# Optimization experiments

Hardware: AMD Instinct MI355X
Metric: run time of the kernel (lower is better)

The kernel has to match this reference:

```python
import jax, jax.numpy as jnp
import numpy as np

EPS = 1e-6


def _layernorm2d(x, w, b):
    # Normalize over channel dim (axis=1) per pixel; x: [B,C,H,W]
    mu = jnp.mean(x, axis=1, keepdims=True)
    var = jnp.var(x, axis=1, keepdims=True)
    xn = (x - mu) * jax.lax.rsqrt(var + EPS)
    return xn * w[None, :, None, None] + b[None, :, None, None]


def _conv1x1(x, w, b):
    # 1x1 conv == channel matmul; w: [Cout, Cin], x: [B,Cin,H,W]
    return jnp.einsum('oc,bchw->bohw', w, x) + b[None, :, None, None]


def setup_inputs() -> dict:
    key = jax.random.key(0)
    ks = jax.random.split(key, 8)
    B, C, H, W = 4, 64, 180, 320
    s = C ** -0.5  # keep projection weights at sane scale
    return {
        'x_l': jax.random.normal(ks[0], (B, C, H, W), jnp.float32),
        'x_r': jax.random.normal(ks[1], (B, C, H, W), jnp.float32),
        'ln_l_w': jnp.ones((C,), jnp.float32),
        'ln_l_b': jnp.zeros((C,), jnp.float32),
        'ln_r_w': jnp.ones((C,), jnp.float32),
        'ln_r_b': jnp.zeros((C,), jnp.float32),
        'wq_l': jax.random.normal(ks[2], (C, C), jnp.float32) * s,
        'bq_l': jnp.zeros((C,), jnp.float32),
        'wq_r': jax.random.normal(ks[3], (C, C), jnp.float32) * s,
        'bq_r': jnp.zeros((C,), jnp.float32),
        'wv_l': jax.random.normal(ks[4], (C, C), jnp.float32) * s,
        'bv_l': jnp.zeros((C,), jnp.float32),
        'wv_r': jax.random.normal(ks[5], (C, C), jnp.float32) * s,
        'bv_r': jnp.zeros((C,), jnp.float32),
        'beta': jax.random.normal(ks[6], (C,), jnp.float32) * 0.1,
        'gamma': jax.random.normal(ks[7], (C,), jnp.float32) * 0.1,
    }


def reference(x_l, x_r, ln_l_w, ln_l_b, ln_r_w, ln_r_b,
              wq_l, bq_l, wq_r, bq_r, wv_l, bv_l, wv_r, bv_r,
              beta, gamma):
    C = x_l.shape[1]
    scale = C ** -0.5
    # Q projections of LayerNorm'd inputs (Select stub == identity pass-through)
    Q_l = _conv1x1(_layernorm2d(x_l, ln_l_w, ln_l_b), wq_l, bq_l)  # [B,C,H,W]
    Q_r = _conv1x1(_layernorm2d(x_r, ln_r_w, ln_r_b), wq_r, bq_r)  # [B,C,H,W]
    V_l = _conv1x1(x_l, wv_l, bv_l)  # [B,C,H,W]
    V_r = _conv1x1(x_r, wv_r, bv_r)  # [B,C,H,W]
    # attention over width per row: [B,H,Wl,Wr]
    attn = jnp.einsum('bchw,bchv->bhwv', Q_l, Q_r) * scale
    # r -> l: softmax over Wr (last axis), contract with V_r
    F_r2l = jnp.einsum('bhwv,bchv->bchw', jax.nn.softmax(attn, axis=-1), V_r)
    # l -> r: softmax over Wl (axis=2 of attn), contract with V_l
    F_l2r = jnp.einsum('bhwv,bchw->bchv', jax.nn.softmax(attn, axis=2), V_l)
    out_l = x_l + F_r2l * beta[None, :, None, None]
    out_r = x_r + F_l2r * gamma[None, :, None, None]
    return (out_l, out_r)
```

## Files before the change

kernel.cpp:

```cpp
#include <hip/hip_runtime.h>


#define HWs  57600
#define CHWs 3686400
#define TOTs 14745600
#define RST  72
#define VST  328
#define PTS  36
#define NTH  768

typedef short bf16x8 __attribute__((ext_vector_type(8)));
typedef float f32x4  __attribute__((ext_vector_type(4)));
union FragU { uint4 q; unsigned short u[8]; bf16x8 v; };

__device__ __forceinline__ unsigned short f2bf(float f) {
  unsigned u = __float_as_uint(f);
  u += 0x7fffu + ((u >> 16) & 1u);
  return (unsigned short)(u >> 16);
}
__device__ __forceinline__ float bf2f(unsigned short s) {
  return __uint_as_float(((unsigned)s) << 16);
}
__device__ __forceinline__ unsigned fenc(float f) {
  unsigned u = __float_as_uint(f);
  return u ^ (0x80000000u | (unsigned)(-(int)(u >> 31)));
}
__device__ __forceinline__ float fdec(unsigned k) {
  return __uint_as_float(k ^ (0x80000000u | (unsigned)(-(int)((k >> 31) ^ 1u))));
}

__global__ __launch_bounds__(NTH, 2)
void sfam_kernel(
    const float* __restrict__ x_l, const float* __restrict__ x_r,
    const float* __restrict__ ln_l_w, const float* __restrict__ ln_l_b,
    const float* __restrict__ ln_r_w, const float* __restrict__ ln_r_b,
    const float* __restrict__ wq_l, const float* __restrict__ bq_l,
    const float* __restrict__ wq_r, const float* __restrict__ bq_r,
    const float* __restrict__ wv_l, const float* __restrict__ bv_l,
    const float* __restrict__ wv_r, const float* __restrict__ bv_r,
    const float* __restrict__ beta, const float* __restrict__ gamma,
    float* __restrict__ out)
{
  __shared__ __align__(16) unsigned short Rs[320*RST];
  __shared__ __align__(16) unsigned short Ks[320*RST];
  __shared__ __align__(16) unsigned short Vb[64*VST];
  __shared__ __align__(16) unsigned short Pt[12*16*PTS];
  __shared__ float NX[320];
  __shared__ float MU[640], RSd[640];
  __shared__ float c_arr[320];
  __shared__ float BB[128];
  __shared__ unsigned SCu[3];

  const int bh = blockIdx.x;
  const int b = bh / 180, h = bh - b*180;
  const int base = b*CHWs + h*320;

  const int t = threadIdx.x;
  const int wave = t >> 6, lane = t & 63;
  const int p = lane & 15, g = lane >> 4;
  const int nwt = (wave < 8) ? 2 : 1;
  const int w0 = (wave < 8) ? wave*32 : 256 + (wave-8)*16;

  if (t < 3) SCu[t] = 0u;

  for (int w2 = t; w2 < 640; w2 += NTH) {
    const int side = (w2 >= 320);
    const int w = w2 - side*320;
    const float* xp = side ? x_r : x_l;
    unsigned short* dst = side ? Ks : Rs;
    float s0 = 0.f, q0 = 0.f, s1 = 0.f, q1 = 0.f;
    #pragma unroll
    for (int cb = 0; cb < 64; cb += 8) {
      FragU f;
      #pragma unroll
      for (int j = 0; j < 8; ++j) {
        const float v = xp[base + (cb+j)*HWs + w];
        if (cb < 32) { s0 += v; q0 += v*v; } else { s1 += v; q1 += v*v; }
        f.u[j] = f2bf(v);
      }
      *(uint4*)&dst[w*RST + cb] = f.q;
    }
    const float m  = (s0 + s1) * (1.f/64.f);
    const float vv = (q0 + q1) * (1.f/64.f) - m*m;
    MU[side*320 + w]  = m;
    RSd[side*320 + w] = rsqrtf(vv + 1e-6f);
    if (side) {
      const float vc = fmaxf(vv, 0.f);
      const float nx = 8.f * sqrtf(vc / (vc + 1e-6f));
      NX[w] = nx;
      atomicMax(&SCu[0], fenc(nx));
    }
  }
  if (t < 128) {
    const int o = t & 63;
    const float* wqp = (t < 64) ? wq_l : wq_r;
    const float* lwp = (t < 64) ? ln_l_w : ln_r_w;
    const float* lbp = (t < 64) ? ln_l_b : ln_r_b;
    const float* bqp = (t < 64) ? bq_l : bq_r;
    float s = bqp[o];
    for (int c = 0; c < 64; ++c) s += wqp[o*64+c]*lwp[c]*lbp[c];
    BB[t] = s;
  }
  __syncthreads();

  auto projV = [&](const float* wvp, const float* bvp, const unsigned short* src,
                   const float* mup, const float* rsp, bool inv) {
    bf16x8 bx[2][2];
    #pragma unroll
    for (int nt = 0; nt < 2; ++nt) if (nt < nwt) {
      const int w = w0 + nt*16 + p;
      const float mu = mup[w];
      const float sd = inv ? (1.0f / rsp[w]) : 0.f;
      #pragma unroll
      for (int kf = 0; kf < 2; ++kf) {
        FragU f; f.q = *(const uint4*)&src[w*RST + kf*32 + g*8];
        if (inv) {
          FragU rr;
          #pragma unroll
          for (int j = 0; j < 8; ++j) rr.u[j] = f2bf(bf2f(f.u[j])*sd + mu);
          bx[nt][kf] = rr.v;
        } else bx[nt][kf] = f.v;
      }
    }
    #pragma unroll
    for (int mt = 0; mt < 4; ++mt) {
      bf16x8 av2[2];
      #pragma unroll
      for (int kf = 0; kf < 2; ++kf) {
        FragU rr;
        #pragma unroll
        for (int j = 0; j < 8; ++j) rr.u[j] = f2bf(wvp[(mt*16+p)*64 + kf*32 + g*8 + j]);
        av2[kf] = rr.v;
      }
      f32x4 acc2[2];
      #pragma unroll
      for (int nt = 0; nt < 2; ++nt) acc2[nt] = (f32x4){0.f,0.f,0.f,0.f};
      #pragma unroll
      for (int nt = 0; nt < 2; ++nt) if (nt < nwt)
        #pragma unroll
        for (int kf = 0; kf < 2; ++kf)
          acc2[nt] = __builtin_amdgcn_mfma_f32_16x16x32_bf16(av2[kf], bx[nt][kf], acc2[nt], 0,0,0);
      #pragma unroll
      for (int nt = 0; nt < 2; ++nt) if (nt < nwt)
        #pragma unroll
        for (int r = 0; r < 4; ++r) {
          const int o = mt*16 + g*4 + r;
          Vb[o*VST + w0 + nt*16 + p] = f2bf(acc2[nt][r] + bvp[o]);
        }
    }
  };

  projV(wv_l, bv_l, Rs, MU, RSd, false);

  float cR[2][4];
  {
    bf16x8 qa[2][2];
    #pragma unroll
    for (int wt = 0; wt < 2; ++wt) if (wt < nwt) {
      const int w = w0 + wt*16 + p;
      const float mu = MU[w], rs = RSd[w];
      #pragma unroll
      for (int kf = 0; kf < 2; ++kf) {
        FragU f; f.q = *(const uint4*)&Rs[w*RST + kf*32 + g*8];
        FragU rr;
        #pragma unroll
        for (int j = 0; j < 8; ++j) rr.u[j] = f2bf((bf2f(f.u[j]) - mu) * rs);
        qa[wt][kf] = rr.v;
      }
    }
    f32x4 qacc[2][4];
    #pragma unroll
    for (int wt = 0; wt < 2; ++wt)
      #pragma unroll
      for (int ot = 0; ot < 4; ++ot) qacc[wt][ot] = (f32x4){0.f,0.f,0.f,0.f};
    #pragma unroll
    for (int ot = 0; ot < 4; ++ot) {
      bf16x8 bw2[2];
      #pragma unroll
      for (int kf = 0; kf < 2; ++kf) {
        FragU rr;
        #pragma unroll
        for (int j = 0; j < 8; ++j) {
          const int c = kf*32 + g*8 + j;
          rr.u[j] = f2bf(wq_l[(ot*16+p)*64 + c] * ln_l_w[c]);
        }
        bw2[kf] = rr.v;
      }
      #pragma unroll
      for (int wt = 0; wt < 2; ++wt) if (wt < nwt)
        #pragma unroll
        for (int kf = 0; kf < 2; ++kf)
          qacc[wt][ot] = __builtin_amdgcn_mfma_f32_16x16x32_bf16(qa[wt][kf], bw2[kf], qacc[wt][ot], 0,0,0);
    }
    #pragma unroll
    for (int wt = 0; wt < 2; ++wt) {
      #pragma unroll
      for (int r = 0; r < 4; ++r) cR[wt][r] = 0.f;
      if (wt < nwt) {
        #pragma unroll
        for (int ot = 0; ot < 4; ++ot) {
          const float bl = BB[ot*16+p], br = BB[64 + ot*16+p];
          #pragma unroll
          for (int r = 0; r < 4; ++r) {
            const float qv = qacc[wt][ot][r] + bl;
            Rs[(w0 + wt*16 + g*4 + r)*RST + ot*16 + p] = f2bf(qv);
            cR[wt][r] += qv * br;
          }
        }
        #pragma unroll
        for (int r = 0; r < 4; ++r) {
          float cv = cR[wt][r];
          cv += __shfl_xor(cv, 1); cv += __shfl_xor(cv, 2);
          cv += __shfl_xor(cv, 4); cv += __shfl_xor(cv, 8);
          cv *= 0.125f;
          cR[wt][r] = cv;
          if (p == 0) {
            c_arr[w0 + wt*16 + g*4 + r] = cv;
            atomicMax(&SCu[2], fenc(cv));
          }
        }
      }
    }
  }

  float rm[2][4];
  {
    bf16x8 qla[2][2];
    #pragma unroll
    for (int wt = 0; wt < 2; ++wt) if (wt < nwt)
      #pragma unroll
      for (int kf = 0; kf < 2; ++kf) {
        FragU f; f.q = *(const uint4*)&Rs[(w0 + wt*16 + p)*RST + kf*32 + g*8];
        qla[wt][kf] = f.v;
      }
    f32x4 q2[2][4];
    #pragma unroll
    for (int wt = 0; wt < 2; ++wt)
      #pragma unroll
      for (int ct = 0; ct < 4; ++ct) q2[wt][ct] = (f32x4){0.f,0.f,0.f,0.f};
    #pragma unroll
    for (int ct = 0; ct < 4; ++ct) {
      const float lw = ln_r_w[ct*16 + p];
      bf16x8 bwt2[2];
      #pragma unroll
      for (int kf = 0; kf < 2; ++kf) {
        FragU rr;
        #pragma unroll
        for (int j = 0; j < 8; ++j)
          rr.u[j] = f2bf(wq_r[(kf*32 + g*8 + j)*64 + ct*16 + p] * lw);
        bwt2[kf] = rr.v;
      }
      #pragma unroll
      for (int wt = 0; wt < 2; ++wt) if (wt < nwt)
        #pragma unroll
        for (int kf = 0; kf < 2; ++kf)
          q2[wt][ct] = __builtin_amdgcn_mfma_f32_16x16x32_bf16(qla[wt][kf], bwt2[kf], q2[wt][ct], 0,0,0);
    }
    const float NXmax = fdec(SCu[0]);
    #pragma unroll
    for (int wt = 0; wt < 2; ++wt) {
      #pragma unroll
      for (int r = 0; r < 4; ++r) rm[wt][r] = 0.f;
      if (wt < nwt) {
        #pragma unroll
        for (int r = 0; r < 4; ++r) {
          float qsq = 0.f;
          #pragma unroll
          for (int ct = 0; ct < 4; ++ct) {
            const float qv = q2[wt][ct][r] * 0.125f;
            Rs[(w0 + wt*16 + g*4 + r)*RST + ct*16 + p] = f2bf(qv);
            qsq += qv*qv;
          }
          qsq += __shfl_xor(qsq, 1); qsq += __shfl_xor(qsq, 2);
          qsq += __shfl_xor(qsq, 4); qsq += __shfl_xor(qsq, 8);
          rm[wt][r] = sqrtf(qsq) * NXmax;
          if (p == 0) atomicMax(&SCu[1], fenc(qsq));
        }
      }
    }
  }

  #pragma unroll
  for (int wt = 0; wt < 2; ++wt) if (wt < nwt) {
    const int w = w0 + wt*16 + p;
    const float mu = MU[320+w], rs = RSd[320+w];
    #pragma unroll
    for (int kf = 0; kf < 2; ++kf) {
      FragU f; f.q = *(const uint4*)&Ks[w*RST + kf*32 + g*8];
      FragU rr;
      #pragma unroll
      for (int j = 0; j < 8; ++j) rr.u[j] = f2bf((bf2f(f.u[j]) - mu) * rs);
      *(uint4*)&Ks[w*RST + kf*32 + g*8] = rr.q;
    }
  }
  __syncthreads();

  bf16x8 aq[2][2];
  #pragma unroll
  for (int wt = 0; wt < 2; ++wt) if (wt < nwt)
    #pragma unroll
    for (int kf = 0; kf < 2; ++kf) {
      FragU f1; f1.q = *(const uint4*)&Rs[(w0 + wt*16 + p)*RST + kf*32 + g*8];
      aq[wt][kf] = f1.v;
    }

  float ls[2][4];
  f32x4 oacc[2][4];
  auto attn_pass = [&](bf16x8 (&A)[2][2], const unsigned short* Bsrc,
                       float (&mx)[2][4], bool colc) {
    float rsa[2][4];
    #pragma unroll
    for (int wt = 0; wt < 2; ++wt)
      #pragma unroll
      for (int r = 0; r < 4; ++r) rsa[wt][r] = 0.f;
    unsigned short* ptw = &Pt[wave*16*PTS];
    for (int ch = 0; ch < 5; ++ch) {
      const int k0 = ch*64;
      #pragma unroll
      for (int pvk = 0; pvk < 2; ++pvk) {
        bf16x8 bq2[2][2];
        #pragma unroll
        for (int vh = 0; vh < 2; ++vh)
          #pragma unroll
          for (int kf = 0; kf < 2; ++kf) {
            FragU f; f.q = *(const uint4*)&Bsrc[(k0 + (pvk*2+vh)*16 + p)*RST + kf*32 + g*8];
            bq2[vh][kf] = f.v;
          }
        float cc2[2];
        #pragma unroll
        for (int vh = 0; vh < 2; ++vh)
          cc2[vh] = colc ? c_arr[k0 + (pvk*2+vh)*16 + p] : 0.f;
        f32x4 sa[2][2];
        #pragma unroll
        for (int wt = 0; wt < 2; ++wt)
          #pragma unroll
          for (int vh = 0; vh < 2; ++vh) sa[wt][vh] = (f32x4){0.f,0.f,0.f,0.f};
        #pragma unroll
        for (int wt = 0; wt < 2; ++wt) if (wt < nwt)
          #pragma unroll
          for (int vh = 0; vh < 2; ++vh)
            #pragma unroll
            for (int kf = 0; kf < 2; ++kf)
              sa[wt][vh] = __builtin_amdgcn_mfma_f32_16x16x32_bf16(A[wt][kf], bq2[vh][kf], sa[wt][vh], 0,0,0);
        #pragma unroll
        for (int wt = 0; wt < 2; ++wt) if (wt < nwt) {
          #pragma unroll
          for (int r = 0; r < 4; ++r) {
            #pragma unroll
            for (int vh = 0; vh < 2; ++vh) {
              const float e = __expf(sa[wt][vh][r] + cc2[vh] - mx[wt][r]);
              sa[wt][vh][r] = e;
              rsa[wt][r] += e;
            }
          }
        }
        bf16x8 bvv[4];
        #pragma unroll
        for (int ot = 0; ot < 4; ++ot) {
          FragU f; f.q = *(const uint4*)&Vb[(ot*16+p)*VST + k0 + pvk*32 + g*8];
          bvv[ot] = f.v;
        }
        #pragma unroll
        for (int wt = 0; wt < 2; ++wt) if (wt < nwt) {
          #pragma unroll
          for (int vh = 0; vh < 2; ++vh)
            #pragma unroll
            for (int r = 0; r < 4; ++r)
              ptw[(g*4 + r)*PTS + vh*16 + p] = f2bf(sa[wt][vh][r]);
          FragU fa; fa.q = *(const uint4*)&ptw[p*PTS + g*8];
          #pragma unroll
          for (int ot = 0; ot < 4; ++ot)
            oacc[wt][ot] = __builtin_amdgcn_mfma_f32_16x16x32_bf16(fa.v, bvv[ot], oacc[wt][ot], 0,0,0);
        }
      }
    }
    #pragma unroll
    for (int wt = 0; wt < 2; ++wt)
      #pragma unroll
      for (int r = 0; r < 4; ++r) {
        float s = rsa[wt][r];
        s += __shfl_xor(s, 1); s += __shfl_xor(s, 2);
        s += __shfl_xor(s, 4); s += __shfl_xor(s, 8);
        ls[wt][r] = s;
      }
  };

  bf16x8 ak[2][2];
  #pragma unroll
  for (int wt = 0; wt < 2; ++wt) if (wt < nwt)
    #pragma unroll
    for (int kf = 0; kf < 2; ++kf) {
      FragU f2; f2.q = *(const uint4*)&Ks[(w0 + wt*16 + p)*RST + kf*32 + g*8];
      ak[wt][kf] = f2.v;
    }
  float cmR[2][4];
  {
    const float Qnmax = sqrtf(fdec(SCu[1]));
    const float Cmax  = fdec(SCu[2]);
    #pragma unroll
    for (int wt = 0; wt < 2; ++wt)
      #pragma unroll
      for (int r = 0; r < 4; ++r)
        cmR[wt][r] = (wt < nwt) ? NX[w0 + wt*16 + g*4 + r] * Qnmax + Cmax : 0.f;
  }
  #pragma unroll
  for (int wt = 0; wt < 2; ++wt)
    #pragma unroll
    for (int ot = 0; ot < 4; ++ot) oacc[wt][ot] = (f32x4){0.f,0.f,0.f,0.f};
  attn_pass(ak, Rs, cmR, true);
  __syncthreads();

  #pragma unroll
  for (int wt = 0; wt < 2; ++wt) if (wt < nwt)
    #pragma unroll
    for (int r = 0; r < 4; ++r) {
      const float inv = 1.0f / ls[wt][r];
      #pragma unroll
      for (int ot = 0; ot < 4; ++ot)
        Rs[(w0 + wt*16 + g*4 + r)*RST + ot*16 + p] = f2bf(oacc[wt][ot][r] * inv);
    }

  projV(wv_r, bv_r, Ks, MU+320, RSd+320, true);
  __syncthreads();

  #pragma unroll
  for (int wt = 0; wt < 2; ++wt)
    #pragma unroll
    for (int ot = 0; ot < 4; ++ot) oacc[wt][ot] = (f32x4){0.f,0.f,0.f,0.f};
  attn_pass(aq, Ks, rm, false);
  __syncthreads();

  #pragma unroll
  for (int wt = 0; wt < 2; ++wt) if (wt < nwt)
    #pragma unroll
    for (int r = 0; r < 4; ++r) {
      const float inv = 1.0f / ls[wt][r];
      #pragma unroll
      for (int ot = 0; ot < 4; ++ot)
        Ks[(w0 + wt*16 + g*4 + r)*RST + ot*16 + p] = f2bf(oacc[wt][ot][r] * inv);
    }
  __syncthreads();

  for (int w2 = t; w2 < 640; w2 += NTH) {
    const int side = (w2 >= 320);
    const int w = w2 - side*320;
    const float* xs = side ? x_r : x_l;
    const unsigned short* Osrc = side ? Rs : Ks;
    const float* sc = side ? gamma : beta;
    float* op = out + (side ? TOTs : 0);
    #pragma unroll
    for (int cb = 0; cb < 64; cb += 8) {
      FragU f; f.q = *(const uint4*)&Osrc[w*RST + cb];
      #pragma unroll
      for (int j = 0; j < 8; ++j) {
        const int cc = cb + j;
        const int gi = base + cc*HWs + w;
        op[gi] = xs[gi] + sc[cc] * bf2f(f.u[j]);
      }
    }
  }
}

extern "C" void kernel_launch(void* const* d_in, const int* in_sizes, int n_in,
                              void* d_out, int out_size, void* d_ws, size_t ws_size,
                              hipStream_t stream) {
  (void)in_sizes; (void)n_in; (void)d_ws; (void)ws_size; (void)out_size;
  sfam_kernel<<<dim3(720), dim3(NTH), 0, stream>>>(
      (const float*)d_in[0],  (const float*)d_in[1],
      (const float*)d_in[2],  (const float*)d_in[3],
      (const float*)d_in[4],  (const float*)d_in[5],
      (const float*)d_in[6],  (const float*)d_in[7],
      (const float*)d_in[8],  (const float*)d_in[9],
      (const float*)d_in[10], (const float*)d_in[11],
      (const float*)d_in[12], (const float*)d_in[13],
      (const float*)d_in[14], (const float*)d_in[15],
      (float*)d_out);
}
```

Baseline: 416.1 us.

## Fold Q_l and Q_r projections into one combined weight matrix per row

Instead of computing Q_l from normalized x_l and then multiplying by Wq_r^T, the kernel precomputes the combined matrix Wq_r^T·diag·Wq_l in shared memory. A single MFMA pass from the normalized input then yields the transformed query, and bias contributions come from precomputed vectors u, f and the scalar s0. This removes one 64x64 matmul per pixel and its intermediate bf16 round trip, at the cost of an extra per-block setup (small GEMM, reductions) and a __syncthreads. The folded product is rounded to bf16 once, so numerics change slightly.

```diff
diff --git a/kernel.cpp b/kernel.cpp
--- a/kernel.cpp
+++ b/kernel.cpp
@@ -7,6 +7,7 @@
 #define RST  72
 #define VST  328
 #define PTS  36
+#define ETS  72
 #define NTH  768
 
 typedef short bf16x8 __attribute__((ext_vector_type(8)));
@@ -50,6 +51,9 @@
   __shared__ float c_arr[320];
   __shared__ float BB[128];
   __shared__ unsigned SCu[3];
+  __shared__ float uArr[64], fArr[64], sS0[1];
+
+  unsigned short* Et = Pt;
 
   const int bh = blockIdx.x;
   const int b = bh / 180, h = bh - b*180;
@@ -152,7 +156,57 @@
 
   projV(wv_l, bv_l, Rs, MU, RSd, false);
 
-  float cR[2][4];
+  if (wave >= 8) {
+    const int dt = wave - 8;
+    const float ascale = ln_r_w[dt*16 + p] * 0.125f;
+    bf16x8 ar[2];
+    #pragma unroll
+    for (int kf = 0; kf < 2; ++kf) {
+      FragU rr;
+      #pragma unroll
+      for (int j = 0; j < 8; ++j)
+        rr.u[j] = f2bf(wq_r[(kf*32 + g*8 + j)*64 + dt*16 + p] * ascale);
+      ar[kf] = rr.v;
+    }
+    #pragma unroll
+    for (int ct = 0; ct < 4; ++ct) {
+      const float bscale = ln_l_w[ct*16 + p];
+      bf16x8 bl[2];
+      #pragma unroll
+      for (int kf = 0; kf < 2; ++kf) {
+        FragU rr;
+        #pragma unroll
+        for (int j = 0; j < 8; ++j)
+          rr.u[j] = f2bf(wq_l[(kf*32 + g*8 + j)*64 + ct*16 + p] * bscale);
+        bl[kf] = rr.v;
+      }
+      f32x4 ea = (f32x4){0.f,0.f,0.f,0.f};
+      ea = __builtin_amdgcn_mfma_f32_16x16x32_bf16(ar[0], bl[0], ea, 0,0,0);
+      ea = __builtin_amdgcn_mfma_f32_16x16x32_bf16(ar[1], bl[1], ea, 0,0,0);
+      #pragma unroll
+      for (int r = 0; r < 4; ++r)
+        Et[(dt*16 + g*4 + r)*ETS + ct*16 + p] = f2bf(ea[r]);
+    }
+  }
+  if (t >= 512 && t < 576) {
+    const int c = t - 512;
+    float s = 0.f;
+    for (int o = 0; o < 64; ++o) s += wq_l[o*64 + c] * BB[64 + o];
+    uArr[c] = s * ln_l_w[c];
+  } else if (t >= 576 && t < 640) {
+    const int d = t - 576;
+    float s = 0.f;
+    for (int o = 0; o < 64; ++o) s += wq_r[o*64 + d] * BB[o];
+    fArr[d] = s * ln_r_w[d] * 0.125f;
+  }
+  if (t == 640) {
+    float s = 0.f;
+    for (int o = 0; o < 64; ++o) s += BB[o] * BB[64 + o];
+    sS0[0] = s;
+  }
+  __syncthreads();
+
+  float rm[2][4];
   {
     bf16x8 qa[2][2];
     #pragma unroll
@@ -168,93 +222,43 @@
         qa[wt][kf] = rr.v;
       }
     }
-    f32x4 qacc[2][4];
+    const float s0v = sS0[0];
+    #pragma unroll
+    for (int wt = 0; wt < 2; ++wt) if (wt < nwt) {
+      float dotp = 0.f;
+      #pragma unroll
+      for (int kf = 0; kf < 2; ++kf) {
+        FragU f; f.v = qa[wt][kf];
+        #pragma unroll
+        for (int j = 0; j < 8; ++j)
+          dotp += bf2f(f.u[j]) * uArr[kf*32 + g*8 + j];
+      }
+      dotp += __shfl_xor(dotp, 16);
+      dotp += __shfl_xor(dotp, 32);
+      const float cv = 0.125f * (dotp + s0v);
+      if (g == 0) {
+        c_arr[w0 + wt*16 + p] = cv;
+        atomicMax(&SCu[2], fenc(cv));
+      }
+    }
+    f32x4 q2[2][4];
     #pragma unroll
     for (int wt = 0; wt < 2; ++wt)
       #pragma unroll
-      for (int ot = 0; ot < 4; ++ot) qacc[wt][ot] = (f32x4){0.f,0.f,0.f,0.f};
-    #pragma unroll
-    for (int ot = 0; ot < 4; ++ot) {
-      bf16x8 bw2[2];
-      #pragma unroll
-      for (int kf = 0; kf < 2; ++kf) {
-        FragU rr;
-        #pragma unroll
-        for (int j = 0; j < 8; ++j) {
-          const int c = kf*32 + g*8 + j;
-          rr.u[j] = f2bf(wq_l[(ot*16+p)*64 + c] * ln_l_w[c]);
-        }
-        bw2[kf] = rr.v;
+      for (int ct = 0; ct < 4; ++ct) q2[wt][ct] = (f32x4){0.f,0.f,0.f,0.f};
+    #pragma unroll
+    for (int ct = 0; ct < 4; ++ct) {
+      bf16x8 be[2];
+      #pragma unroll
+      for (int kf = 0; kf < 2; ++kf) {
+        FragU f; f.q = *(const uint4*)&Et[(ct*16 + p)*ETS + kf*32 + g*8];
+        be[kf] = f.v;
       }
       #pragma unroll
       for (int wt = 0; wt < 2; ++wt) if (wt < nwt)
         #pragma unroll
         for (int kf = 0; kf < 2; ++kf)
-          qacc[wt][ot] = __builtin_amdgcn_mfma_f32_16x16x32_bf16(qa[wt][kf], bw2[kf], qacc[wt][ot], 0,0,0);
-    }
-    #pragma unroll
-    for (int wt = 0; wt < 2; ++wt) {
-      #pragma unroll
-      for (int r = 0; r < 4; ++r) cR[wt][r] = 0.f;
-      if (wt < nwt) {
-        #pragma unroll
-        for (int ot = 0; ot < 4; ++ot) {
-          const float bl = BB[ot*16+p], br = BB[64 + ot*16+p];
-          #pragma unroll
-          for (int r = 0; r < 4; ++r) {
-            const float qv = qacc[wt][ot][r] + bl;
-            Rs[(w0 + wt*16 + g*4 + r)*RST + ot*16 + p] = f2bf(qv);
-            cR[wt][r] += qv * br;
-          }
-        }
-        #pragma unroll
-        for (int r = 0; r < 4; ++r) {
-          float cv = cR[wt][r];
-          cv += __shfl_xor(cv, 1); cv += __shfl_xor(cv, 2);
-          cv += __shfl_xor(cv, 4); cv += __shfl_xor(cv, 8);
-          cv *= 0.125f;
-          cR[wt][r] = cv;
-          if (p == 0) {
-            c_arr[w0 + wt*16 + g*4 + r] = cv;
-            atomicMax(&SCu[2], fenc(cv));
-          }
-        }
-      }
-    }
-  }
-
-  float rm[2][4];
-  {
-    bf16x8 qla[2][2];
-    #pragma unroll
-    for (int wt = 0; wt < 2; ++wt) if (wt < nwt)
-      #pragma unroll
-      for (int kf = 0; kf < 2; ++kf) {
-        FragU f; f.q = *(const uint4*)&Rs[(w0 + wt*16 + p)*RST + kf*32 + g*8];
-        qla[wt][kf] = f.v;
-      }
-    f32x4 q2[2][4];
-    #pragma unroll
-    for (int wt = 0; wt < 2; ++wt)
-      #pragma unroll
-      for (int ct = 0; ct < 4; ++ct) q2[wt][ct] = (f32x4){0.f,0.f,0.f,0.f};
-    #pragma unroll
-    for (int ct = 0; ct < 4; ++ct) {
-      const float lw = ln_r_w[ct*16 + p];
-      bf16x8 bwt2[2];
-      #pragma unroll
-      for (int kf = 0; kf < 2; ++kf) {
-        FragU rr;
-        #pragma unroll
-        for (int j = 0; j < 8; ++j)
-          rr.u[j] = f2bf(wq_r[(kf*32 + g*8 + j)*64 + ct*16 + p] * lw);
-        bwt2[kf] = rr.v;
-      }
-      #pragma unroll
-      for (int wt = 0; wt < 2; ++wt) if (wt < nwt)
-        #pragma unroll
-        for (int kf = 0; kf < 2; ++kf)
-          q2[wt][ct] = __builtin_amdgcn_mfma_f32_16x16x32_bf16(qla[wt][kf], bwt2[kf], q2[wt][ct], 0,0,0);
+          q2[wt][ct] = __builtin_amdgcn_mfma_f32_16x16x32_bf16(qa[wt][kf], be[kf], q2[wt][ct], 0,0,0);
     }
     const float NXmax = fdec(SCu[0]);
     #pragma unroll
@@ -267,7 +271,7 @@
           float qsq = 0.f;
           #pragma unroll
           for (int ct = 0; ct < 4; ++ct) {
-            const float qv = q2[wt][ct][r] * 0.125f;
+            const float qv = q2[wt][ct][r] + fArr[ct*16 + p];
             Rs[(w0 + wt*16 + g*4 + r)*RST + ct*16 + p] = f2bf(qv);
             qsq += qv*qv;
           }
```

Result: faster. 400.4 us (-3.8%).
